# Performance work log

Hardware: AMD Instinct MI355X
Metric: run time of the kernel (lower is better)

The kernel has to match this reference:

```python
import jax, jax.numpy as jnp
import numpy as np


def setup_inputs() -> dict:
    key = jax.random.key(0)
    k1, k2 = jax.random.split(key)
    B, Te, Td, D = 16, 1024, 1024, 1024
    encoder_outputs = jax.random.normal(k1, (B, Te, D), dtype=jnp.float32)
    decoder_outputs = jax.random.normal(k2, (B, Td, D), dtype=jnp.float32)
    return {"encoder_outputs": encoder_outputs, "decoder_outputs": decoder_outputs}


def reference(encoder_outputs, decoder_outputs):
    # Luong score: [B, Te, Td] = enc @ dec^T
    luong_score = jnp.einsum("bed,btd->bet", encoder_outputs, decoder_outputs)
    # softmax over encoder-time axis (axis=1), matching K.softmax(..., axis=1)
    attn = jax.nn.softmax(luong_score, axis=1)
    # context vector: sum over encoder time of enc * attn -> [B, Td, D]
    # (original materializes [B, Te, Td, D]; this einsum is the same math)
    encoder_vector = jnp.einsum("bed,bet->btd", encoder_outputs, attn)
    return jnp.concatenate([decoder_outputs, encoder_vector], axis=-1)
```

## Files before the change

kernel.cpp:

```cpp
#include <hip/hip_runtime.h>
#include <hip/hip_bf16.h>
#include <stdint.h>

typedef __bf16 bf16x8 __attribute__((ext_vector_type(8)));
typedef float f32x4 __attribute__((ext_vector_type(4)));

#define B_DIM 16
#define TD 1024
#define TE 1024
#define DD 1024

typedef __attribute__((address_space(1))) void as1_void;
typedef __attribute__((address_space(3))) void as3_void;

#define GLL16(gp, lp) \
  __builtin_amdgcn_global_load_lds((as1_void*)(gp), (as3_void*)(lp), 16, 0, 0)

#define SB __builtin_amdgcn_sched_barrier(0)
#define BAR()                      \
  do {                             \
    SB;                            \
    __builtin_amdgcn_s_barrier();  \
    SB;                            \
  } while (0)
#define VMW4()                                       \
  do {                                               \
    asm volatile("s_waitcnt vmcnt(4)" ::: "memory"); \
    SB;                                              \
  } while (0)

__device__ __forceinline__ uint32_t rne_bf16(float x) {
  uint32_t u = __builtin_bit_cast(uint32_t, x);
  return (u + 0x7FFFu + ((u >> 16) & 1u)) >> 16;
}

__device__ __forceinline__ void split2(float x, uint32_t& hi, uint32_t& lo) {
  uint32_t h = rne_bf16(x);
  float hf = __builtin_bit_cast(float, h << 16);
  hi = h;
  lo = rne_bf16(x - hf);
}

__global__ __launch_bounds__(256)
void p0a_split_dec(const float4* __restrict__ dec4, uint32_t* __restrict__ dhi,
                   uint32_t* __restrict__ dlo) {
  size_t g = (size_t)blockIdx.x * 256 + threadIdx.x;
#pragma unroll
  for (int s = 0; s < 8; ++s, g += 524288) {
    float4 v = dec4[g];
    uint32_t h0, l0, h1, l1, h2, l2, h3, l3;
    split2(v.x, h0, l0);
    split2(v.y, h1, l1);
    split2(v.z, h2, l2);
    split2(v.w, h3, l3);
    *(uint2*)&dhi[g * 2] = make_uint2(h0 | (h1 << 16), h2 | (h3 << 16));
    *(uint2*)&dlo[g * 2] = make_uint2(l0 | (l1 << 16), l2 | (l3 << 16));
  }
}

__global__ __launch_bounds__(256)
void p0b_split_enc(const float* __restrict__ enc, uint32_t* __restrict__ ehi,
                   uint32_t* __restrict__ elo, uint16_t* __restrict__ eT) {
  __shared__ uint16_t TT[64][65];
  const int tid = threadIdx.x;
  const int b = blockIdx.z;
  const int d0 = (blockIdx.x & 15) * 64, e0 = (blockIdx.x >> 4) * 64;
  const float* src = enc + (size_t)b * TE * DD;
#pragma unroll
  for (int s = 0; s < 4; ++s) {
    int c = tid + 256 * s;
    int row = c >> 4, c4 = c & 15;
    float4 v = *(const float4*)(src + (size_t)(e0 + row) * DD + d0 + c4 * 4);
    uint32_t h0, l0, h1, l1, h2, l2, h3, l3;
    split2(v.x, h0, l0);
    split2(v.y, h1, l1);
    split2(v.z, h2, l2);
    split2(v.w, h3, l3);
    size_t o = (((size_t)b * TE + e0 + row) * DD + d0 + c4 * 4) >> 1;
    *(uint2*)&ehi[o] = make_uint2(h0 | (h1 << 16), h2 | (h3 << 16));
    *(uint2*)&elo[o] = make_uint2(l0 | (l1 << 16), l2 | (l3 << 16));
    TT[row][c4 * 4 + 0] = (uint16_t)h0;
    TT[row][c4 * 4 + 1] = (uint16_t)h1;
    TT[row][c4 * 4 + 2] = (uint16_t)h2;
    TT[row][c4 * 4 + 3] = (uint16_t)h3;
  }
  __syncthreads();
#pragma unroll
  for (int s = 0; s < 4; ++s) {
    int c = tid + 256 * s;
    int d = c >> 4, e4 = c & 15;
    uint32_t w0 = (uint32_t)TT[e4 * 4 + 0][d] | ((uint32_t)TT[e4 * 4 + 1][d] << 16);
    uint32_t w1 = (uint32_t)TT[e4 * 4 + 2][d] | ((uint32_t)TT[e4 * 4 + 3][d] << 16);
    *(uint2*)&eT[((size_t)b * DD + d0 + d) * TE + e0 + e4 * 4] = make_uint2(w0, w1);
  }
}

template <int NSEG>
__global__ __launch_bounds__(512, 2)
void k_gemm256(const uint16_t* __restrict__ a0, const uint16_t* __restrict__ a1,
               const uint16_t* __restrict__ a2, const uint16_t* __restrict__ b0,
               const uint16_t* __restrict__ b1, const uint16_t* __restrict__ b2,
               float* __restrict__ out) {
  extern __shared__ char lds[];
  const int tid = threadIdx.x;
  const int lane = tid & 63, wave = tid >> 6;
  const int wr = wave >> 2, wc = wave & 3;
  const int lr = lane & 15, q = lane >> 4;

  const int id = blockIdx.x;
  const int swz = (id & 7) * 32 + (id >> 3);
  const int b = swz >> 4, mblk = (swz >> 2) & 3, nblk = swz & 3;
  const size_t bOff = (size_t)b << 20;
  const uint16_t* As0 = a0 + bOff;
  const uint16_t* As1 = a1 + bOff;
  const uint16_t* As2 = a2 + bOff;
  const uint16_t* Bs0 = b0 + bOff;
  const uint16_t* Bs1 = b1 + bOff;
  const uint16_t* Bs2 = b2 + bOff;
  const int mrow0 = mblk * 256, nrow0 = nblk * 256;
  constexpr int T = NSEG * 16;

  f32x4 acc[8][4] = {};
  bf16x8 a[8], bA[2], bB[2];

  auto STAGE = [&](int op, int half, int tau, int buf) {
    int seg, klt;
    if constexpr (NSEG == 3) {
      seg = tau >> 4;
      klt = tau & 15;
    } else {
      seg = 0;
      klt = tau;
    }
    const uint16_t* base;
    if (op == 0)
      base = (seg == 0) ? As0 : ((seg == 1) ? As1 : As2);
    else
      base = (seg == 0) ? Bs0 : ((seg == 1) ? Bs1 : Bs2);
    base += (size_t)((op == 0 ? mrow0 : nrow0) + half * 128) * 1024 + klt * 64;
    char* dst = lds + (((buf * 2 + op) * 2 + half) << 14);
#pragma unroll
    for (int j = 0; j < 2; ++j) {
      int chunk = j * 512 + tid;
      int row = chunk >> 3;
      int k8 = ((chunk & 7) ^ (row & 7)) << 3;
      GLL16(base + (size_t)row * 1024 + k8, dst + chunk * 16);
    }
  };

  auto LDA = [&](int kk, int buf) {
    const char* src = lds + (((buf * 2 + 0) * 2 + wr) << 14);
#pragma unroll
    for (int mi = 0; mi < 8; ++mi) {
      int rl = mi * 16 + lr;
      int col = (kk * 64 + q * 16) ^ ((rl & 7) << 4);
      a[mi] = *(const bf16x8*)(src + rl * 128 + col);
    }
  };
  auto LDB = [&](int kk, int nbase, bf16x8* bb, int buf) {
    const char* src = lds + (((buf * 2 + 1) * 2 + (wc >> 1)) << 14);
#pragma unroll
    for (int u = 0; u < 2; ++u) {
      int rl = (wc & 1) * 64 + (nbase + u) * 16 + lr;
      int col = (kk * 64 + q * 16) ^ ((rl & 7) << 4);
      bb[u] = *(const bf16x8*)(src + rl * 128 + col);
    }
  };
  auto MFMAQ = [&](bf16x8* bb, int npair) {
#pragma unroll
    for (int u = 0; u < 2; ++u)
#pragma unroll
      for (int mi = 0; mi < 8; ++mi)
        acc[mi][npair * 2 + u] = __builtin_amdgcn_mfma_f32_16x16x32_bf16(
            a[mi], bb[u], acc[mi][npair * 2 + u], 0, 0, 0);
  };

  STAGE(0, 0, 0, 0);
  STAGE(0, 1, 0, 0);
  STAGE(1, 0, 0, 0);
  STAGE(1, 1, 0, 0);
  STAGE(0, 0, 1, 1);
  STAGE(0, 1, 1, 1);
  VMW4();
  BAR();

  for (int t = 0; t < T; ++t) {
    const int cur = t & 1, nxt = cur ^ 1;
    const int t1 = (t + 1 < T) ? t + 1 : 0;
    const int t2 = (t + 2 < T) ? t + 2 : t + 2 - T;
    LDA(0, cur);
    LDB(0, 0, bA, cur);
    STAGE(1, 0, t1, nxt);
    BAR();
    __builtin_amdgcn_s_setprio(1);
    MFMAQ(bA, 0);
    __builtin_amdgcn_s_setprio(0);
    BAR();
    LDB(0, 2, bB, cur);
    STAGE(1, 1, t1, nxt);
    BAR();
    __builtin_amdgcn_s_setprio(1);
    MFMAQ(bB, 1);
    __builtin_amdgcn_s_setprio(0);
    BAR();
    LDA(1, cur);
    LDB(1, 2, bB, cur);
    BAR();
    __builtin_amdgcn_s_setprio(1);
    MFMAQ(bB, 1);
    __builtin_amdgcn_s_setprio(0);
    BAR();
    LDB(1, 0, bA, cur);
    STAGE(0, 0, t2, cur);
    STAGE(0, 1, t2, cur);
    VMW4();
    BAR();
    __builtin_amdgcn_s_setprio(1);
    MFMAQ(bA, 0);
    __builtin_amdgcn_s_setprio(0);
    BAR();
  }

  float* outp = out + (size_t)b * TD * 2048 + 1024;
  const int m0 = mrow0 + wr * 128 + q * 4;
  const int n0 = nrow0 + wc * 64 + lr;
#pragma unroll
  for (int mi = 0; mi < 8; ++mi)
#pragma unroll
    for (int ni = 0; ni < 4; ++ni)
#pragma unroll
      for (int i = 0; i < 4; ++i)
        outp[(size_t)(m0 + mi * 16 + i) * 2048 + (n0 + ni * 16)] = acc[mi][ni][i];
}

__global__ __launch_bounds__(256)
void k2_softmax_v2(const float* __restrict__ dec, float* __restrict__ out,
                   uint16_t* __restrict__ P) {
  const int lane = threadIdx.x & 63;
  const int row = blockIdx.x * 4 + (threadIdx.x >> 6);
  const float* Srow = out + (size_t)row * 2048 + 1024;
  float4 v[4];
#pragma unroll
  for (int s = 0; s < 4; ++s) v[s] = *(const float4*)(Srow + lane * 4 + s * 256);
  float m = -1e30f;
#pragma unroll
  for (int s = 0; s < 4; ++s)
    m = fmaxf(m, fmaxf(fmaxf(v[s].x, v[s].y), fmaxf(v[s].z, v[s].w)));
#pragma unroll
  for (int o = 32; o > 0; o >>= 1) m = fmaxf(m, __shfl_xor(m, o));
  float e[16];
  float sum = 0.f;
#pragma unroll
  for (int s = 0; s < 4; ++s) {
    e[4 * s + 0] = __expf(v[s].x - m);
    e[4 * s + 1] = __expf(v[s].y - m);
    e[4 * s + 2] = __expf(v[s].z - m);
    e[4 * s + 3] = __expf(v[s].w - m);
    sum += e[4 * s + 0] + e[4 * s + 1] + e[4 * s + 2] + e[4 * s + 3];
  }
#pragma unroll
  for (int o = 32; o > 0; o >>= 1) sum += __shfl_xor(sum, o);
  const float inv = 1.0f / sum;
  uint32_t* Prow = (uint32_t*)(P + (size_t)row * 1024);
#pragma unroll
  for (int s = 0; s < 4; ++s) {
    uint32_t r0 = rne_bf16(e[4 * s + 0] * inv);
    uint32_t r1 = rne_bf16(e[4 * s + 1] * inv);
    uint32_t r2 = rne_bf16(e[4 * s + 2] * inv);
    uint32_t r3 = rne_bf16(e[4 * s + 3] * inv);
    *(uint2*)&Prow[lane * 2 + s * 128] =
        make_uint2(r0 | (r1 << 16), r2 | (r3 << 16));
  }
  const float4* d4 = (const float4*)(dec + (size_t)row * 1024);
  float4* o4 = (float4*)(out + (size_t)row * 2048);
#pragma unroll
  for (int s = 0; s < 4; ++s) o4[lane + s * 64] = d4[lane + s * 64];
}

__global__ __launch_bounds__(256, 2)
void k1_scores(const float* __restrict__ dec, const float* __restrict__ enc,
               float* __restrict__ out) {
  __shared__ uint32_t AhU[2048], AlU[2048], BhU[2048], BlU[2048];
  const int tid = threadIdx.x;
  const int lane = tid & 63;
  const int wave = tid >> 6;
  const int wm = wave >> 1, wn = wave & 1;
  const int b = blockIdx.z;
  const int t0 = blockIdx.y * 128, e0 = blockIdx.x * 128;
  const float* A = dec + (size_t)b * TD * DD;
  const float* Bm = enc + (size_t)b * TE * DD;

  const int r = tid >> 3, c4 = tid & 7;
  const float* aptr = A + (size_t)(t0 + r) * DD + c4 * 4;
  const float* bptr = Bm + (size_t)(e0 + r) * DD + c4 * 4;

  const int lr = lane & 15, q = lane >> 4;
  int aoff[4], boff[4];
#pragma unroll
  for (int i = 0; i < 4; ++i) {
    aoff[i] = (wm * 64 + i * 16 + lr) * 16 + q * 4;
    boff[i] = (wn * 64 + i * 16 + lr) * 16 + q * 4;
  }

  f32x4 acc[4][4] = {};

  for (int k0 = 0; k0 < DD; k0 += 32) {
#pragma unroll
    for (int s = 0; s < 4; ++s) {
      const float4 va = *(const float4*)(aptr + (size_t)(32 * s) * DD);
      const float4 vb = *(const float4*)(bptr + (size_t)(32 * s) * DD);
      const int woff = (r + 32 * s) * 16 + c4 * 2;
      {
        uint32_t u0 = __builtin_bit_cast(uint32_t, va.x);
        uint32_t u1 = __builtin_bit_cast(uint32_t, va.y);
        uint32_t u2 = __builtin_bit_cast(uint32_t, va.z);
        uint32_t u3 = __builtin_bit_cast(uint32_t, va.w);
        uint32_t m0 = u0 & 0xFFFF0000u, m1 = u1 & 0xFFFF0000u;
        uint32_t m2 = u2 & 0xFFFF0000u, m3 = u3 & 0xFFFF0000u;
        float l0 = va.x - __builtin_bit_cast(float, m0);
        float l1 = va.y - __builtin_bit_cast(float, m1);
        float l2 = va.z - __builtin_bit_cast(float, m2);
        float l3 = va.w - __builtin_bit_cast(float, m3);
        *(uint2*)&AhU[woff] = make_uint2((m0 >> 16) | m1, (m2 >> 16) | m3);
        *(uint2*)&AlU[woff] = make_uint2(
            (__builtin_bit_cast(uint32_t, l0) >> 16) |
                (__builtin_bit_cast(uint32_t, l1) & 0xFFFF0000u),
            (__builtin_bit_cast(uint32_t, l2) >> 16) |
                (__builtin_bit_cast(uint32_t, l3) & 0xFFFF0000u));
      }
      {
        uint32_t u0 = __builtin_bit_cast(uint32_t, vb.x);
        uint32_t u1 = __builtin_bit_cast(uint32_t, vb.y);
        uint32_t u2 = __builtin_bit_cast(uint32_t, vb.z);
        uint32_t u3 = __builtin_bit_cast(uint32_t, vb.w);
        uint32_t m0 = u0 & 0xFFFF0000u, m1 = u1 & 0xFFFF0000u;
        uint32_t m2 = u2 & 0xFFFF0000u, m3 = u3 & 0xFFFF0000u;
        float l0 = vb.x - __builtin_bit_cast(float, m0);
        float l1 = vb.y - __builtin_bit_cast(float, m1);
        float l2 = vb.z - __builtin_bit_cast(float, m2);
        float l3 = vb.w - __builtin_bit_cast(float, m3);
        *(uint2*)&BhU[woff] = make_uint2((m0 >> 16) | m1, (m2 >> 16) | m3);
        *(uint2*)&BlU[woff] = make_uint2(
            (__builtin_bit_cast(uint32_t, l0) >> 16) |
                (__builtin_bit_cast(uint32_t, l1) & 0xFFFF0000u),
            (__builtin_bit_cast(uint32_t, l2) >> 16) |
                (__builtin_bit_cast(uint32_t, l3) & 0xFFFF0000u));
      }
    }
    __syncthreads();

    bf16x8 ah[4], al[4];
#pragma unroll
    for (int mi = 0; mi < 4; ++mi) {
      ah[mi] = *(const bf16x8*)&AhU[aoff[mi]];
      al[mi] = *(const bf16x8*)&AlU[aoff[mi]];
    }
#pragma unroll
    for (int ni = 0; ni < 4; ++ni) {
      bf16x8 bh = *(const bf16x8*)&BhU[boff[ni]];
      bf16x8 bl = *(const bf16x8*)&BlU[boff[ni]];
#pragma unroll
      for (int mi = 0; mi < 4; ++mi) {
        f32x4 c = acc[mi][ni];
        c = __builtin_amdgcn_mfma_f32_16x16x32_bf16(al[mi], bh, c, 0, 0, 0);
        c = __builtin_amdgcn_mfma_f32_16x16x32_bf16(ah[mi], bl, c, 0, 0, 0);
        c = __builtin_amdgcn_mfma_f32_16x16x32_bf16(ah[mi], bh, c, 0, 0, 0);
        acc[mi][ni] = c;
      }
    }
    __syncthreads();
    aptr += 32;
    bptr += 32;
  }

  float* outb = out + (size_t)b * TD * 2048 + 1024;
  const int tb = t0 + wm * 64 + q * 4;
  const int eb = e0 + wn * 64 + lr;
#pragma unroll
  for (int mi = 0; mi < 4; ++mi)
#pragma unroll
    for (int ni = 0; ni < 4; ++ni)
#pragma unroll
      for (int i = 0; i < 4; ++i)
        outb[(size_t)(tb + mi * 16 + i) * 2048 + (eb + ni * 16)] = acc[mi][ni][i];
}

__global__ __launch_bounds__(256)
void k2_softmax(float* out) {
  const int lane = threadIdx.x & 63;
  const int row = blockIdx.x * 4 + (threadIdx.x >> 6);
  float* Srow = out + (size_t)row * 2048 + 1024;
  float4 v[4];
#pragma unroll
  for (int s = 0; s < 4; ++s) v[s] = *(const float4*)(Srow + lane * 4 + s * 256);
  float m = -1e30f;
#pragma unroll
  for (int s = 0; s < 4; ++s)
    m = fmaxf(m, fmaxf(fmaxf(v[s].x, v[s].y), fmaxf(v[s].z, v[s].w)));
#pragma unroll
  for (int o = 32; o > 0; o >>= 1) m = fmaxf(m, __shfl_xor(m, o));
  float e[16];
  float sum = 0.f;
#pragma unroll
  for (int s = 0; s < 4; ++s) {
    e[4 * s + 0] = __expf(v[s].x - m);
    e[4 * s + 1] = __expf(v[s].y - m);
    e[4 * s + 2] = __expf(v[s].z - m);
    e[4 * s + 3] = __expf(v[s].w - m);
    sum += e[4 * s + 0] + e[4 * s + 1] + e[4 * s + 2] + e[4 * s + 3];
  }
#pragma unroll
  for (int o = 32; o > 0; o >>= 1) sum += __shfl_xor(sum, o);
  const float inv = 1.0f / sum;
  uint32_t* Prow = (uint32_t*)(out + (size_t)row * 2048);
#pragma unroll
  for (int s = 0; s < 4; ++s) {
    uint32_t r0 = rne_bf16(e[4 * s + 0] * inv);
    uint32_t r1 = rne_bf16(e[4 * s + 1] * inv);
    uint32_t r2 = rne_bf16(e[4 * s + 2] * inv);
    uint32_t r3 = rne_bf16(e[4 * s + 3] * inv);
    *(uint2*)&Prow[lane * 2 + s * 128] =
        make_uint2(r0 | (r1 << 16), r2 | (r3 << 16));
  }
}

__global__ __launch_bounds__(256, 2)
void k3_av(const float* __restrict__ enc, float* __restrict__ out) {
  __shared__ uint32_t AU[2048];
  __shared__ uint32_t BtU[128 * 20];
  const int tid = threadIdx.x;
  const int lane = tid & 63, wave = tid >> 6;
  const int wm = wave >> 1, wn = wave & 1;
  const int b = blockIdx.z;
  const int t0 = blockIdx.y * 128, d0 = blockIdx.x * 128;
  const float* V = enc + (size_t)b * TE * DD;
  const uint16_t* Pb = (const uint16_t*)(out + (size_t)b * TD * 2048);
  const int lr = lane & 15, q = lane >> 4;
  int aoff[4], boff[4];
#pragma unroll
  for (int i = 0; i < 4; ++i) {
    aoff[i] = (wm * 64 + i * 16 + lr) * 16 + q * 4;
    boff[i] = (wn * 64 + i * 16 + lr) * 20 + q * 4;
  }
  const int dB = tid & 127;
  f32x4 acc[4][4] = {};

  for (int e0k = 0; e0k < TE; e0k += 32) {
#pragma unroll
    for (int s = 0; s < 2; ++s) {
      int c = tid + 256 * s;
      int rc = c >> 2, cc = c & 3;
      uint4 va = *(const uint4*)(Pb + (size_t)(t0 + rc) * 4096 + e0k + cc * 8);
      *(uint4*)&AU[c * 4] = va;
    }
#pragma unroll
    for (int s = 0; s < 4; ++s) {
      int eg = (tid >> 7) + 2 * s;
      const float* src = V + (size_t)(e0k + eg * 4) * DD + d0 + dB;
      float x0 = src[0], x1 = src[DD], x2 = src[2 * DD], x3 = src[3 * DD];
      uint32_t r0 = rne_bf16(x0), r1 = rne_bf16(x1);
      uint32_t r2 = rne_bf16(x2), r3 = rne_bf16(x3);
      *(uint2*)&BtU[dB * 20 + eg * 2] =
          make_uint2(r0 | (r1 << 16), r2 | (r3 << 16));
    }
    __syncthreads();

    bf16x8 af[4];
#pragma unroll
    for (int mi = 0; mi < 4; ++mi) af[mi] = *(const bf16x8*)&AU[aoff[mi]];
#pragma unroll
    for (int ni = 0; ni < 4; ++ni) {
      bf16x8 bfr = *(const bf16x8*)&BtU[boff[ni]];
#pragma unroll
      for (int mi = 0; mi < 4; ++mi)
        acc[mi][ni] =
            __builtin_amdgcn_mfma_f32_16x16x32_bf16(af[mi], bfr, acc[mi][ni], 0, 0, 0);
    }
    __syncthreads();
  }

  float* outb = out + (size_t)b * TD * 2048 + 1024;
  const int tb = t0 + wm * 64 + q * 4;
  const int db = d0 + wn * 64 + lr;
#pragma unroll
  for (int mi = 0; mi < 4; ++mi)
#pragma unroll
    for (int ni = 0; ni < 4; ++ni)
#pragma unroll
      for (int i = 0; i < 4; ++i)
        outb[(size_t)(tb + mi * 16 + i) * 2048 + (db + ni * 16)] = acc[mi][ni][i];
}

__global__ __launch_bounds__(256)
void k4_copydec(const float4* __restrict__ dec4, float4* __restrict__ out4) {
  size_t g = (size_t)blockIdx.x * 512 + threadIdx.x;
#pragma unroll
  for (int s = 0; s < 2; ++s, g += 256) {
    size_t row = g >> 8, col = g & 255;
    out4[row * 512 + col] = dec4[g];
  }
}

extern "C" void kernel_launch(void* const* d_in, const int* in_sizes, int n_in,
                              void* d_out, int out_size, void* d_ws, size_t ws_size,
                              hipStream_t stream) {
  const float* enc = (const float*)d_in[0];
  const float* dec = (const float*)d_in[1];
  float* out = (float*)d_out;

  const size_t M32 = 32ull << 20;
  bool fast = (d_ws != nullptr) && (ws_size >= 5 * M32);
  if (fast) {
    hipError_t e1 = hipFuncSetAttribute(
        (const void*)k_gemm256<3>, hipFuncAttributeMaxDynamicSharedMemorySize,
        131072);
    hipError_t e2 = hipFuncSetAttribute(
        (const void*)k_gemm256<1>, hipFuncAttributeMaxDynamicSharedMemorySize,
        131072);
    if (e1 != hipSuccess || e2 != hipSuccess) fast = false;
  }

  if (fast) {
    char* ws = (char*)d_ws;
    uint16_t* dhi = (uint16_t*)(ws);
    uint16_t* dlo = (uint16_t*)(ws + M32);
    uint16_t* ehi = (uint16_t*)(ws + 2 * M32);
    uint16_t* elo = (uint16_t*)(ws + 3 * M32);
    uint16_t* eT = (uint16_t*)(ws + 4 * M32);
    uint16_t* P = dhi;

    hipLaunchKernelGGL(p0a_split_dec, dim3(2048), dim3(256), 0, stream,
                       (const float4*)dec, (uint32_t*)dhi, (uint32_t*)dlo);
    hipLaunchKernelGGL(p0b_split_enc, dim3(256, 1, 16), dim3(256), 0, stream,
                       enc, (uint32_t*)ehi, (uint32_t*)elo, eT);
    hipLaunchKernelGGL(k_gemm256<3>, dim3(256), dim3(512), 131072, stream,
                       dhi, dhi, dlo, ehi, elo, ehi, out);
    hipLaunchKernelGGL(k2_softmax_v2, dim3(4096), dim3(256), 0, stream, dec, out, P);
    hipLaunchKernelGGL(k_gemm256<1>, dim3(256), dim3(512), 131072, stream,
                       P, P, P, eT, eT, eT, out);
  } else {
    hipLaunchKernelGGL(k1_scores, dim3(8, 8, 16), dim3(256), 0, stream, dec, enc, out);
    hipLaunchKernelGGL(k2_softmax, dim3(4096), dim3(256), 0, stream, out);
    hipLaunchKernelGGL(k3_av, dim3(8, 8, 16), dim3(256), 0, stream, enc, out);
    hipLaunchKernelGGL(k4_copydec, dim3(8192), dim3(256), 0, stream,
                       (const float4*)dec, (float4*)out);
  }
}
```

Before: 410.9 us.

## Fuse decoder copy into split kernel and precompute GEMM LDS/global addresses

Moves the copy of decoder_outputs into the output's first half out of the softmax kernel and into the decoder split kernel, which already reads dec, so dec is loaded once instead of twice. The GEMM's staging and LDS-read address math is replaced by per-thread base pointers that toggle between the two buffers each iteration. The loop also reorders the LDS fragment loads, fetching both B pairs up front for each k-half, which raises register pressure. The loop is kept rolled with unroll 1.

Result: faster. 400.6 us (-2.5%).

```diff
diff --git a/kernel.cpp b/kernel.cpp
--- a/kernel.cpp
+++ b/kernel.cpp
@@ -43,7 +43,7 @@
 
 __global__ __launch_bounds__(256)
 void p0a_split_dec(const float4* __restrict__ dec4, uint32_t* __restrict__ dhi,
-                   uint32_t* __restrict__ dlo) {
+                   uint32_t* __restrict__ dlo, float4* __restrict__ out4) {
   size_t g = (size_t)blockIdx.x * 256 + threadIdx.x;
 #pragma unroll
   for (int s = 0; s < 8; ++s, g += 524288) {
@@ -55,6 +55,8 @@
     split2(v.w, h3, l3);
     *(uint2*)&dhi[g * 2] = make_uint2(h0 | (h1 << 16), h2 | (h3 << 16));
     *(uint2*)&dlo[g * 2] = make_uint2(l0 | (l1 << 16), l2 | (l3 << 16));
+    size_t row = g >> 8, col = g & 255;
+    out4[row * 512 + col] = v;
   }
 }
 
@@ -111,61 +113,55 @@
   const int swz = (id & 7) * 32 + (id >> 3);
   const int b = swz >> 4, mblk = (swz >> 2) & 3, nblk = swz & 3;
   const size_t bOff = (size_t)b << 20;
-  const uint16_t* As0 = a0 + bOff;
-  const uint16_t* As1 = a1 + bOff;
-  const uint16_t* As2 = a2 + bOff;
-  const uint16_t* Bs0 = b0 + bOff;
-  const uint16_t* Bs1 = b1 + bOff;
-  const uint16_t* Bs2 = b2 + bOff;
   const int mrow0 = mblk * 256, nrow0 = nblk * 256;
   constexpr int T = NSEG * 16;
 
+  const uint16_t* aS0 = a0 + bOff + (size_t)mrow0 * 1024;
+  const uint16_t* aS1 = a1 + bOff + (size_t)mrow0 * 1024;
+  const uint16_t* aS2 = a2 + bOff + (size_t)mrow0 * 1024;
+  const uint16_t* bS0 = b0 + bOff + (size_t)nrow0 * 1024;
+  const uint16_t* bS1 = b1 + bOff + (size_t)nrow0 * 1024;
+  const uint16_t* bS2 = b2 + bOff + (size_t)nrow0 * 1024;
+
+  const int r8 = tid >> 3, c8 = tid & 7;
+  const int laneOff = r8 * 1024 + ((c8 ^ (r8 & 7)) << 3);
+  char* dTid = lds + tid * 16;
+
+#define STAGE_OP(P0_, P1_, P2_, HALF_, TAU_, REGION_)                         \
+  do {                                                                        \
+    int sg_ = (NSEG == 3) ? ((TAU_) >> 4) : 0;                                \
+    int kl_ = (TAU_) & 15;                                                    \
+    const uint16_t* s_ =                                                      \
+        ((NSEG == 3) ? (sg_ == 0 ? (P0_) : (sg_ == 1 ? (P1_) : (P2_)))        \
+                     : (P0_)) +                                               \
+        (size_t)(HALF_)*131072 + (kl_ << 6) + laneOff;                        \
+    char* d_ = dTid + (REGION_)*16384;                                        \
+    GLL16(s_, d_);                                                            \
+    GLL16(s_ + 65536, d_ + 8192);                                             \
+  } while (0)
+
+  const int xr = (lr & 7) << 4;
+  const int colx = (q * 16) ^ xr;
+  const char* aRd0 = lds + (wr << 14) + lr * 128 + colx;
+  const char* aRd1 = lds + (wr << 14) + lr * 128 + (colx ^ 64);
+  const char* bRdB = lds + ((2 + (wc >> 1)) << 14) + (wc & 1) * 8192 + lr * 128;
+  const char* bRd0 = bRdB + colx;
+  const char* bRd1 = bRdB + (colx ^ 64);
+
   f32x4 acc[8][4] = {};
   bf16x8 a[8], bA[2], bB[2];
 
-  auto STAGE = [&](int op, int half, int tau, int buf) {
-    int seg, klt;
-    if constexpr (NSEG == 3) {
-      seg = tau >> 4;
-      klt = tau & 15;
-    } else {
-      seg = 0;
-      klt = tau;
-    }
-    const uint16_t* base;
-    if (op == 0)
-      base = (seg == 0) ? As0 : ((seg == 1) ? As1 : As2);
-    else
-      base = (seg == 0) ? Bs0 : ((seg == 1) ? Bs1 : Bs2);
-    base += (size_t)((op == 0 ? mrow0 : nrow0) + half * 128) * 1024 + klt * 64;
-    char* dst = lds + (((buf * 2 + op) * 2 + half) << 14);
-#pragma unroll
-    for (int j = 0; j < 2; ++j) {
-      int chunk = j * 512 + tid;
-      int row = chunk >> 3;
-      int k8 = ((chunk & 7) ^ (row & 7)) << 3;
-      GLL16(base + (size_t)row * 1024 + k8, dst + chunk * 16);
-    }
-  };
-
-  auto LDA = [&](int kk, int buf) {
-    const char* src = lds + (((buf * 2 + 0) * 2 + wr) << 14);
-#pragma unroll
-    for (int mi = 0; mi < 8; ++mi) {
-      int rl = mi * 16 + lr;
-      int col = (kk * 64 + q * 16) ^ ((rl & 7) << 4);
-      a[mi] = *(const bf16x8*)(src + rl * 128 + col);
-    }
-  };
-  auto LDB = [&](int kk, int nbase, bf16x8* bb, int buf) {
-    const char* src = lds + (((buf * 2 + 1) * 2 + (wc >> 1)) << 14);
-#pragma unroll
-    for (int u = 0; u < 2; ++u) {
-      int rl = (wc & 1) * 64 + (nbase + u) * 16 + lr;
-      int col = (kk * 64 + q * 16) ^ ((rl & 7) << 4);
-      bb[u] = *(const bf16x8*)(src + rl * 128 + col);
-    }
-  };
+#define LDA_ALL(SRC_)                                    \
+  do {                                                   \
+    _Pragma("unroll") for (int mi = 0; mi < 8; ++mi)     \
+        a[mi] = *(const bf16x8*)((SRC_) + mi * 2048);    \
+  } while (0)
+#define LDB2(SRC_, NB_, DST_)                               \
+  do {                                                      \
+    DST_[0] = *(const bf16x8*)((SRC_) + (NB_)*2048);        \
+    DST_[1] = *(const bf16x8*)((SRC_) + ((NB_) + 1) * 2048);\
+  } while (0)
+
   auto MFMAQ = [&](bf16x8* bb, int npair) {
 #pragma unroll
     for (int u = 0; u < 2; ++u)
@@ -175,51 +171,61 @@
             a[mi], bb[u], acc[mi][npair * 2 + u], 0, 0, 0);
   };
 
-  STAGE(0, 0, 0, 0);
-  STAGE(0, 1, 0, 0);
-  STAGE(1, 0, 0, 0);
-  STAGE(1, 1, 0, 0);
-  STAGE(0, 0, 1, 1);
-  STAGE(0, 1, 1, 1);
+  STAGE_OP(aS0, aS1, aS2, 0, 0, 0);
+  STAGE_OP(aS0, aS1, aS2, 1, 0, 1);
+  STAGE_OP(bS0, bS1, bS2, 0, 0, 2);
+  STAGE_OP(bS0, bS1, bS2, 1, 0, 3);
+  STAGE_OP(aS0, aS1, aS2, 0, 1, 4);
+  STAGE_OP(aS0, aS1, aS2, 1, 1, 5);
   VMW4();
   BAR();
 
+  int dir = 65536;
+#pragma unroll 1
   for (int t = 0; t < T; ++t) {
     const int cur = t & 1, nxt = cur ^ 1;
-    const int t1 = (t + 1 < T) ? t + 1 : 0;
+    const int t1 = (t + 1 < T) ? t + 1 : t + 1 - T;
     const int t2 = (t + 2 < T) ? t + 2 : t + 2 - T;
-    LDA(0, cur);
-    LDB(0, 0, bA, cur);
-    STAGE(1, 0, t1, nxt);
+    LDA_ALL(aRd0);
+    LDB2(bRd0, 0, bA);
+    LDB2(bRd0, 2, bB);
+    STAGE_OP(bS0, bS1, bS2, 0, t1, nxt * 4 + 2);
     BAR();
     __builtin_amdgcn_s_setprio(1);
     MFMAQ(bA, 0);
     __builtin_amdgcn_s_setprio(0);
     BAR();
-    LDB(0, 2, bB, cur);
-    STAGE(1, 1, t1, nxt);
+    STAGE_OP(bS0, bS1, bS2, 1, t1, nxt * 4 + 3);
     BAR();
     __builtin_amdgcn_s_setprio(1);
     MFMAQ(bB, 1);
     __builtin_amdgcn_s_setprio(0);
     BAR();
-    LDA(1, cur);
-    LDB(1, 2, bB, cur);
+    LDA_ALL(aRd1);
+    LDB2(bRd1, 0, bA);
+    LDB2(bRd1, 2, bB);
     BAR();
     __builtin_amdgcn_s_setprio(1);
     MFMAQ(bB, 1);
     __builtin_amdgcn_s_setprio(0);
     BAR();
-    LDB(1, 0, bA, cur);
-    STAGE(0, 0, t2, cur);
-    STAGE(0, 1, t2, cur);
+    STAGE_OP(aS0, aS1, aS2, 0, t2, cur * 4 + 0);
+    STAGE_OP(aS0, aS1, aS2, 1, t2, cur * 4 + 1);
     VMW4();
     BAR();
     __builtin_amdgcn_s_setprio(1);
     MFMAQ(bA, 0);
     __builtin_amdgcn_s_setprio(0);
     BAR();
-  }
+    aRd0 += dir;
+    aRd1 += dir;
+    bRd0 += dir;
+    bRd1 += dir;
+    dir = -dir;
+  }
+#undef STAGE_OP
+#undef LDA_ALL
+#undef LDB2
 
   float* outp = out + (size_t)b * TD * 2048 + 1024;
   const int m0 = mrow0 + wr * 128 + q * 4;
@@ -234,8 +240,7 @@
 }
 
 __global__ __launch_bounds__(256)
-void k2_softmax_v2(const float* __restrict__ dec, float* __restrict__ out,
-                   uint16_t* __restrict__ P) {
+void k2_softmax_v3(const float* __restrict__ out, uint16_t* __restrict__ P) {
   const int lane = threadIdx.x & 63;
   const int row = blockIdx.x * 4 + (threadIdx.x >> 6);
   const float* Srow = out + (size_t)row * 2048 + 1024;
@@ -271,10 +276,6 @@
     *(uint2*)&Prow[lane * 2 + s * 128] =
         make_uint2(r0 | (r1 << 16), r2 | (r3 << 16));
   }
-  const float4* d4 = (const float4*)(dec + (size_t)row * 1024);
-  float4* o4 = (float4*)(out + (size_t)row * 2048);
-#pragma unroll
-  for (int s = 0; s < 4; ++s) o4[lane + s * 64] = d4[lane + s * 64];
 }
 
 __global__ __launch_bounds__(256, 2)
@@ -530,12 +531,13 @@
     uint16_t* P = dhi;
 
     hipLaunchKernelGGL(p0a_split_dec, dim3(2048), dim3(256), 0, stream,
-                       (const float4*)dec, (uint32_t*)dhi, (uint32_t*)dlo);
+                       (const float4*)dec, (uint32_t*)dhi, (uint32_t*)dlo,
+                       (float4*)out);
     hipLaunchKernelGGL(p0b_split_enc, dim3(256, 1, 16), dim3(256), 0, stream,
                        enc, (uint32_t*)ehi, (uint32_t*)elo, eT);
     hipLaunchKernelGGL(k_gemm256<3>, dim3(256), dim3(512), 131072, stream,
                        dhi, dhi, dlo, ehi, elo, ehi, out);
-    hipLaunchKernelGGL(k2_softmax_v2, dim3(4096), dim3(256), 0, stream, dec, out, P);
+    hipLaunchKernelGGL(k2_softmax_v3, dim3(4096), dim3(256), 0, stream, out, P);
     hipLaunchKernelGGL(k_gemm256<1>, dim3(256), dim3(512), 131072, stream,
                        P, P, P, eT, eT, eT, out);
   } else {
```
